# Kernel optimization log

Measured on AMD Instinct MI355X. Metric: run time of the kernel, lower is better.

The kernel has to match this reference:

```python
import jax, jax.numpy as jnp
import numpy as np


def setup_inputs() -> dict:
    key = jax.random.key(0)
    k1, k2 = jax.random.split(key)
    B, Lc, Lm, D = 8, 2048, 2048, 128
    context = jax.random.normal(k1, (B, Lc, D), dtype=jnp.float32)
    main = jax.random.normal(k2, (B, Lm, D), dtype=jnp.float32)
    return {"context": context, "main": main}


def reference(context, main):
    # weights[b,c,m] = sum_d context[b,c,d] * main[b,m,d]   (Keras dot axes=[2,2])
    weights = jnp.einsum("bcd,bmd->bcm", context, main)
    # K.softmax default axis=-1: normalize over the main-length axis m
    weights = jax.nn.softmax(weights, axis=-1)
    # dot([weights, context], axes=1): contract axis 1 (c) of both -> (B, Lm, D)
    weighted = jnp.einsum("bcm,bcd->bmd", weights, context)
    return main - weighted
```

## Files before the change

### kernel.cpp

```cpp
#include <hip/hip_runtime.h>


#define BATCH 8
#define L_SEQ 2048
#define DD 128
#define SHIFT 40.0f
#define LDA 136

typedef __attribute__((ext_vector_type(8))) short bf16x8;
typedef __attribute__((ext_vector_type(4))) short bf16x4;
typedef __attribute__((ext_vector_type(4))) float f32x4;
typedef __attribute__((ext_vector_type(16))) float f32x16;
typedef __attribute__((ext_vector_type(4))) unsigned int uint4v;

__device__ __forceinline__ short f2bf(float f) {
    unsigned u = __builtin_bit_cast(unsigned, f);
    return (short)((u + 0x8000u) >> 16);
}

__device__ __forceinline__ void gl2lds16(const short* g, short* l) {
    __builtin_amdgcn_global_load_lds(
        (const __attribute__((address_space(1))) unsigned int*)g,
        (__attribute__((address_space(3))) unsigned int*)l, 16, 0, 0);
}

template <int NT>
__device__ __forceinline__ void stage_tile(short* __restrict__ dst,
                                           const float* __restrict__ src,
                                           int nelts, int t) {
    for (int base = 0; base < nelts; base += NT * 8) {
        int flat = base + t * 8;
        const float4* p = (const float4*)(src + flat);
        float4 v0 = p[0];
        float4 v1 = p[1];
        bf16x8 s;
        s[0] = f2bf(v0.x); s[1] = f2bf(v0.y); s[2] = f2bf(v0.z); s[3] = f2bf(v0.w);
        s[4] = f2bf(v1.x); s[5] = f2bf(v1.y); s[6] = f2bf(v1.z); s[7] = f2bf(v1.w);
        int row = flat >> 7;
        int col = flat & 127;
        *(bf16x8*)&dst[row * LDA + col] = s;
    }
}

__global__ __launch_bounds__(256) void zero_kernel(float* __restrict__ p, int n) {
    int i = blockIdx.x * 256 + threadIdx.x;
    if (i < n) p[i] = 0.0f;
}


__global__ __launch_bounds__(256) void convert_kernel(const float* __restrict__ ctx,
                                                      const float* __restrict__ mn,
                                                      short* __restrict__ Cbf,
                                                      short* __restrict__ Mbf,
                                                      float* __restrict__ Lg) {
    int tid = blockIdx.x * 256 + threadIdx.x;
    if (tid < BATCH * L_SEQ) Lg[tid] = 0.0f;
    const int half = BATCH * L_SEQ * DD / 8;
    int id = tid;
    const float* src;
    short* dst;
    if (id < half) { src = ctx; dst = Cbf; }
    else           { id -= half; src = mn; dst = Mbf; }
    int row = id >> 4;
    int lc = id & 15;
    const float4* p = (const float4*)(src + ((size_t)row << 7) + lc * 8);
    float4 v0 = p[0];
    float4 v1 = p[1];
    bf16x8 s;
    s[0] = f2bf(v0.x); s[1] = f2bf(v0.y); s[2] = f2bf(v0.z); s[3] = f2bf(v0.w);
    s[4] = f2bf(v1.x); s[5] = f2bf(v1.y); s[6] = f2bf(v1.z); s[7] = f2bf(v1.w);
    int pc = (lc & 8) | ((lc ^ row) & 7);
    *(bf16x8*)&dst[((size_t)row << 7) + pc * 8] = s;
}

__global__ __launch_bounds__(256, 2) void stats_kernel(const short* __restrict__ Cbf,
                                                       const short* __restrict__ Mbf,
                                                       float* __restrict__ Lg) {
    __shared__ short Cs[128 * 128];
    __shared__ short Ms[2][64 * 128];

    int bid = blockIdx.x;
    int mc = bid & 3;
    int ct = (bid >> 2) & 15;
    int b  = bid >> 6;
    int t = threadIdx.x;
    int w = t >> 6;
    int l = t & 63;
    int a15 = l & 15;
    int q = l >> 4;
    int h = a15 & 7;
    int cw = (w & 1) * 64;
    int mw = (w >> 1) * 32;

    {
        const short* gC = Cbf + ((size_t)(b * L_SEQ + ct * 128)) * DD;
        const short* gM = Mbf + ((size_t)(b * L_SEQ + mc * 512)) * DD;
        #pragma unroll
        for (int ii = 0; ii < 8; ++ii) {
            int inst = w * 8 + ii;
            gl2lds16(gC + inst * 512 + l * 8, Cs + inst * 512);
        }
        #pragma unroll
        for (int ii = 0; ii < 4; ++ii) {
            int inst = w * 4 + ii;
            gl2lds16(gM + inst * 512 + l * 8, Ms[0] + inst * 512);
        }
    }

    __syncthreads();

    {
        const short* gM = Mbf + ((size_t)(b * L_SEQ + mc * 512 + 64)) * DD;
        #pragma unroll
        for (int ii = 0; ii < 4; ++ii) {
            int inst = w * 4 + ii;
            gl2lds16(gM + inst * 512 + l * 8, Ms[1] + inst * 512);
        }
    }

    bf16x8 af[4][4];
    #pragma unroll
    for (int ks = 0; ks < 4; ++ks) {
        int aoff = ((ks * 4 + q) ^ h) * 8;
        #pragma unroll
        for (int i = 0; i < 4; ++i)
            af[ks][i] = *(const bf16x8*)&Cs[(cw + i * 16 + a15) * 128 + aoff];
    }

    float ls[4][4] = {};

    for (int ms = 0; ms < 8; ++ms) {
        int bp = ms & 1;
        if (ms > 0) {
            __syncthreads();
            if (ms < 7) {
                const short* gM = Mbf + ((size_t)(b * L_SEQ + mc * 512 + (ms + 1) * 64)) * DD;
                #pragma unroll
                for (int ii = 0; ii < 4; ++ii) {
                    int inst = w * 4 + ii;
                    gl2lds16(gM + inst * 512 + l * 8, Ms[bp ^ 1] + inst * 512);
                }
            }
        }

        f32x4 acc[4][2];
        #pragma unroll
        for (int i = 0; i < 4; ++i)
            #pragma unroll
            for (int j = 0; j < 2; ++j) {
                f32x4 z = {0.f, 0.f, 0.f, 0.f};
                acc[i][j] = z;
            }
        #pragma unroll
        for (int ks = 0; ks < 4; ++ks) {
            int aoff = ((ks * 4 + q) ^ h) * 8;
            bf16x8 bv[2];
            #pragma unroll
            for (int j = 0; j < 2; ++j)
                bv[j] = *(const bf16x8*)&Ms[bp][(mw + j * 16 + a15) * 128 + aoff];
            #pragma unroll
            for (int i = 0; i < 4; ++i)
                #pragma unroll
                for (int j = 0; j < 2; ++j)
                    acc[i][j] = __builtin_amdgcn_mfma_f32_16x16x32_bf16(af[ks][i], bv[j], acc[i][j], 0, 0, 0);
        }

        #pragma unroll
        for (int j = 0; j < 2; ++j)
            #pragma unroll
            for (int i = 0; i < 4; ++i)
                #pragma unroll
                for (int r = 0; r < 4; ++r)
                    ls[i][r] += __expf(acc[i][j][r] - SHIFT);
    }

    #pragma unroll
    for (int i = 0; i < 4; ++i)
        #pragma unroll
        for (int r = 0; r < 4; ++r) {
            float v = ls[i][r];
            v += __shfl_xor(v, 1);
            v += __shfl_xor(v, 2);
            v += __shfl_xor(v, 4);
            v += __shfl_xor(v, 8);
            ls[i][r] = v;
        }
    if (a15 == 0) {
        #pragma unroll
        for (int i = 0; i < 4; ++i) {
            int c = ct * 128 + cw + i * 16 + q * 4;
            #pragma unroll
            for (int r = 0; r < 4; ++r)
                atomicAdd(&Lg[(size_t)b * L_SEQ + c + r], ls[i][r]);
        }
    }
}

__global__ __launch_bounds__(256) void prep_kernel(const float* __restrict__ ctx,
                                                   const float* __restrict__ Lg,
                                                   short* __restrict__ CtL) {
    __shared__ short Ts[128 * LDA];
    __shared__ float invLs[128];

    int b = blockIdx.x >> 4;
    int cc = blockIdx.x & 15;
    int t = threadIdx.x;

    if (t < 128) invLs[t] = 1.0f / Lg[(size_t)b * L_SEQ + cc * 128 + t];
    __syncthreads();

    const float* src = ctx + ((size_t)(b * L_SEQ + cc * 128)) * DD;
    #pragma unroll
    for (int i = 0; i < 8; ++i) {
        int flat = i * 2048 + t * 8;
        int r = flat >> 7;
        int c = flat & 127;
        const float4* p = (const float4*)(src + flat);
        float4 v0 = p[0];
        float4 v1 = p[1];
        float il = invLs[r];
        bf16x8 s;
        s[0] = f2bf(v0.x * il); s[1] = f2bf(v0.y * il); s[2] = f2bf(v0.z * il); s[3] = f2bf(v0.w * il);
        s[4] = f2bf(v1.x * il); s[5] = f2bf(v1.y * il); s[6] = f2bf(v1.z * il); s[7] = f2bf(v1.w * il);
        *(bf16x8*)&Ts[r * LDA + c] = s;
    }
    __syncthreads();

    int d = t >> 1;
    int ch = (t & 1) * 64;
    int key = d & 7;
    #pragma unroll
    for (int i = 0; i < 8; ++i) {
        int c = ch + i * 8;
        bf16x8 v;
        #pragma unroll
        for (int j = 0; j < 8; ++j) v[j] = Ts[(c + j) * LDA + d];
        int pc = cc * 16 + (ch >> 3) + (i ^ key);
        *(bf16x8*)&CtL[((size_t)(b * DD + d)) * L_SEQ + pc * 8] = v;
    }
}

__global__ __launch_bounds__(512, 2) void attend_fused(const short* __restrict__ Cbf,
                                                       const short* __restrict__ Mbf,
                                                       const short* __restrict__ CtL,
                                                       const float* __restrict__ mn,
                                                       float* __restrict__ out) {
    __shared__ __align__(16) char smem[131072];

    int bid = blockIdx.x;
    int mtile = bid & 31;
    int b = bid >> 5;
    int t = threadIdx.x;
    int w = t >> 6;
    int l = t & 63;
    int la = l & 31;
    int hi = l >> 5;
    int mg = w >> 2;
    int ch = w & 3;

    int m_glob = mtile * 64 + mg * 32 + la;

    bf16x8 mf[8];
    {
        const short* mrow = Mbf + ((size_t)(b * L_SEQ + m_glob)) * DD;
        int key = m_glob & 7;
        #pragma unroll
        for (int ks = 0; ks < 8; ++ks) {
            int lc = ks * 2 + hi;
            int pc = (lc & 8) | ((lc ^ key) & 7);
            mf[ks] = *(const bf16x8*)&mrow[pc * 8];
        }
    }

    auto stage = [&](int cs, int p) {
        short* Cw = (short*)(smem + p * 65536);
        short* Tw = (short*)(smem + p * 65536 + 32768);
        const short* gC = Cbf + ((size_t)(b * L_SEQ + cs * 128)) * DD;
        #pragma unroll
        for (int ii = 0; ii < 4; ++ii) {
            int inst = w * 4 + ii;
            gl2lds16(gC + inst * 512 + l * 8, Cw + inst * 512);
        }
        const short* gT = CtL + (size_t)b * DD * L_SEQ + (size_t)cs * 128;
        #pragma unroll
        for (int ii = 0; ii < 4; ++ii) {
            int inst = w * 4 + ii;
            int row = inst * 4 + (l >> 4);
            gl2lds16(gT + (size_t)row * L_SEQ + (l & 15) * 8, Tw + inst * 512);
        }
    };

    f32x16 o[4];
    #pragma unroll
    for (int dg = 0; dg < 4; ++dg)
        #pragma unroll
        for (int r = 0; r < 16; ++r) o[dg][r] = 0.0f;

    stage(0, 0);

    for (int cs = 0; cs < 16; ++cs) {
        int p = cs & 1;
        __syncthreads();
        if (cs < 15) stage(cs + 1, p ^ 1);

        const short* Cw = (const short*)(smem + p * 65536);
        const short* Tw = (const short*)(smem + p * 65536 + 32768);

        f32x16 s;
        #pragma unroll
        for (int r = 0; r < 16; ++r) s[r] = 0.0f;
        int crow = ch * 32 + la;
        int ckey = la & 7;
        #pragma unroll
        for (int ks = 0; ks < 8; ++ks) {
            int lc = ks * 2 + hi;
            int pc = (lc & 8) | ((lc ^ ckey) & 7);
            bf16x8 av = *(const bf16x8*)&Cw[crow * 128 + pc * 8];
            s = __builtin_amdgcn_mfma_f32_32x32x16_bf16(av, mf[ks], s, 0, 0, 0);
        }

        unsigned u[4][2];
        #pragma unroll
        for (int q = 0; q < 4; ++q)
            #pragma unroll
            for (int jj = 0; jj < 2; ++jj) {
                float e0 = __expf(s[q * 4 + jj * 2]     - SHIFT);
                float e1 = __expf(s[q * 4 + jj * 2 + 1] - SHIFT);
                u[q][jj] = ((unsigned)(unsigned short)f2bf(e1) << 16)
                         |  (unsigned)(unsigned short)f2bf(e0);
            }

        bf16x8 pa[2];
        #pragma unroll
        for (int ks2 = 0; ks2 < 2; ++ks2) {
            unsigned a0 = u[2 * ks2][0],     a1 = u[2 * ks2][1];
            unsigned b0 = u[2 * ks2 + 1][0], b1 = u[2 * ks2 + 1][1];
            unsigned a0p = (unsigned)__shfl_xor((int)a0, 32);
            unsigned a1p = (unsigned)__shfl_xor((int)a1, 32);
            unsigned b0p = (unsigned)__shfl_xor((int)b0, 32);
            unsigned b1p = (unsigned)__shfl_xor((int)b1, 32);
            uint4v pw;
            pw.x = hi ? b0p : a0;
            pw.y = hi ? b1p : a1;
            pw.z = hi ? b0  : a0p;
            pw.w = hi ? b1  : a1p;
            pa[ks2] = __builtin_bit_cast(bf16x8, pw);
        }

        #pragma unroll
        for (int dg = 0; dg < 4; ++dg) {
            int drow = dg * 32 + la;
            int dkey = drow & 7;
            #pragma unroll
            for (int ks2 = 0; ks2 < 2; ++ks2) {
                int lc2 = ch * 4 + ks2 * 2 + hi;
                int pc2 = (lc2 & 8) | ((lc2 ^ dkey) & 7);
                bf16x8 tv = *(const bf16x8*)&Tw[drow * 128 + pc2 * 8];
                o[dg] = __builtin_amdgcn_mfma_f32_32x32x16_bf16(tv, pa[ks2], o[dg], 0, 0, 0);
            }
        }
    }

    __syncthreads();
    float* red = (float*)smem;
    {
        float* base = red + w * 4096;
        #pragma unroll
        for (int dg = 0; dg < 4; ++dg)
            #pragma unroll
            for (int r = 0; r < 16; ++r) {
                int d = dg * 32 + (r & 3) + 8 * (r >> 2) + 4 * hi;
                base[d * 32 + la] = o[dg][r];
            }
    }
    __syncthreads();

    {
        int mg2 = t >> 8;
        int dq  = (t >> 5) & 7;
        int m   = t & 31;
        int m_out = mtile * 64 + mg2 * 32 + m;
        size_t gbase = ((size_t)(b * L_SEQ + m_out)) * DD + dq * 16;
        const float* r0 = red + (mg2 * 4 + 0) * 4096;
        const float* r1 = red + (mg2 * 4 + 1) * 4096;
        const float* r2 = red + (mg2 * 4 + 2) * 4096;
        const float* r3 = red + (mg2 * 4 + 3) * 4096;
        #pragma unroll
        for (int jq = 0; jq < 4; ++jq) {
            f32x4 v;
            #pragma unroll
            for (int e = 0; e < 4; ++e) {
                int idx = (dq * 16 + jq * 4 + e) * 32 + m;
                v[e] = r0[idx] + r1[idx] + r2[idx] + r3[idx];
            }
            f32x4 mv = *(const f32x4*)&mn[gbase + jq * 4];
            f32x4 ov;
            ov[0] = mv[0] - v[0]; ov[1] = mv[1] - v[1];
            ov[2] = mv[2] - v[2]; ov[3] = mv[3] - v[3];
            *(f32x4*)&out[gbase + jq * 4] = ov;
        }
    }
}


__global__ __launch_bounds__(256, 4) void stats_fb(const float* __restrict__ ctx,
                                                   const float* __restrict__ mn,
                                                   float* __restrict__ Lg) {
    __shared__ short Cs[64 * LDA];
    __shared__ short Ms[64 * LDA];

    int bid = blockIdx.x;
    int mc = bid & 3;
    int ct = (bid >> 2) & 31;
    int b  = bid >> 7;
    int t = threadIdx.x;
    int w = t >> 6;
    int l = t & 63;
    int a15 = l & 15;
    int q = l >> 4;

    stage_tile<256>(Cs, ctx + ((size_t)b * L_SEQ + ct * 64) * DD, 64 * DD, t);

    float ls[4] = {0.f, 0.f, 0.f, 0.f};
    for (int mt = 0; mt < 8; ++mt) {
        __syncthreads();
        int m0 = (mc * 8 + mt) * 64;
        stage_tile<256>(Ms, mn + ((size_t)b * L_SEQ + m0) * DD, 64 * DD, t);
        __syncthreads();

        f32x4 acc[4] = {{0.f,0.f,0.f,0.f},{0.f,0.f,0.f,0.f},{0.f,0.f,0.f,0.f},{0.f,0.f,0.f,0.f}};
        #pragma unroll
        for (int ks = 0; ks < 4; ++ks) {
            int k0 = ks * 32 + q * 8;
            bf16x8 a = *(const bf16x8*)&Cs[(w * 16 + a15) * LDA + k0];
            #pragma unroll
            for (int g = 0; g < 4; ++g) {
                bf16x8 bb = *(const bf16x8*)&Ms[(g * 16 + a15) * LDA + k0];
                acc[g] = __builtin_amdgcn_mfma_f32_16x16x32_bf16(a, bb, acc[g], 0, 0, 0);
            }
        }
        #pragma unroll
        for (int g = 0; g < 4; ++g)
            #pragma unroll
            for (int r = 0; r < 4; ++r)
                ls[r] += __expf(acc[g][r] - SHIFT);
    }

    #pragma unroll
    for (int r = 0; r < 4; ++r) {
        float v = ls[r];
        v += __shfl_xor(v, 1);
        v += __shfl_xor(v, 2);
        v += __shfl_xor(v, 4);
        v += __shfl_xor(v, 8);
        ls[r] = v;
    }
    if (a15 == 0) {
        int c = ct * 64 + w * 16 + q * 4;
        #pragma unroll
        for (int r = 0; r < 4; ++r)
            atomicAdd(&Lg[(size_t)b * L_SEQ + c + r], ls[r]);
    }
}

__global__ __launch_bounds__(1024, 4) void attend_fb(const float* __restrict__ ctx,
                                                     const float* __restrict__ mn,
                                                     const float* __restrict__ Lg,
                                                     float* __restrict__ out) {
    __shared__ short Mt[64 * LDA];
    __shared__ short Cs[128 * LDA];
    __shared__ short Ct[128 * LDA];
    __shared__ short Ps[64 * LDA];
    __shared__ float invLs[128];

    int bid = blockIdx.x;
    int mtile = bid & 31;
    int b = bid >> 5;
    int m0 = mtile * 64;
    int t = threadIdx.x;
    int w = t >> 6;
    int l = t & 63;
    int a15 = l & 15;
    int q = l >> 4;
    int mg = w & 3;
    int pg = w >> 2;

    stage_tile<1024>(Mt, mn + ((size_t)b * L_SEQ + m0) * DD, 64 * DD, t);

    f32x4 oacc[2] = {{0.f,0.f,0.f,0.f},{0.f,0.f,0.f,0.f}};

    for (int cs = 0; cs < 16; ++cs) {
        int c0 = cs * 128;
        __syncthreads();
        stage_tile<1024>(Cs, ctx + ((size_t)b * L_SEQ + c0) * DD, 128 * DD, t);
        if (t < 128) invLs[t] = 1.0f / Lg[(size_t)b * L_SEQ + c0 + t];
        __syncthreads();

        {
            int cc = t & 127;
            int d0 = (t >> 7) * 16;
            #pragma unroll
            for (int hh = 0; hh < 2; ++hh) {
                bf16x8 v = *(const bf16x8*)&Cs[cc * LDA + d0 + hh * 8];
                #pragma unroll
                for (int j = 0; j < 8; ++j)
                    Ct[(d0 + hh * 8 + j) * LDA + cc] = v[j];
            }
        }

        f32x4 sacc[2] = {{0.f,0.f,0.f,0.f},{0.f,0.f,0.f,0.f}};
        #pragma unroll
        for (int ks = 0; ks < 4; ++ks) {
            int k0 = ks * 32 + q * 8;
            bf16x8 a = *(const bf16x8*)&Mt[(mg * 16 + a15) * LDA + k0];
            #pragma unroll
            for (int g = 0; g < 2; ++g) {
                bf16x8 bb = *(const bf16x8*)&Cs[((pg * 2 + g) * 16 + a15) * LDA + k0];
                sacc[g] = __builtin_amdgcn_mfma_f32_16x16x32_bf16(a, bb, sacc[g], 0, 0, 0);
            }
        }
        #pragma unroll
        for (int g = 0; g < 2; ++g) {
            int cl = (pg * 2 + g) * 16 + a15;
            float il = invLs[cl];
            #pragma unroll
            for (int r = 0; r < 4; ++r) {
                float p = __expf(sacc[g][r] - SHIFT) * il;
                Ps[(mg * 16 + q * 4 + r) * LDA + cl] = f2bf(p);
            }
        }
        __syncthreads();

        #pragma unroll
        for (int ks = 0; ks < 4; ++ks) {
            int k0 = ks * 32 + q * 8;
            bf16x8 a = *(const bf16x8*)&Ps[(mg * 16 + a15) * LDA + k0];
            #pragma unroll
            for (int g = 0; g < 2; ++g) {
                bf16x8 bb = *(const bf16x8*)&Ct[((pg * 2 + g) * 16 + a15) * LDA + k0];
                oacc[g] = __builtin_amdgcn_mfma_f32_16x16x32_bf16(a, bb, oacc[g], 0, 0, 0);
            }
        }
    }

    #pragma unroll
    for (int g = 0; g < 2; ++g) {
        int dl = (pg * 2 + g) * 16 + a15;
        #pragma unroll
        for (int r = 0; r < 4; ++r) {
            int ml = mg * 16 + q * 4 + r;
            size_t idx = ((size_t)b * L_SEQ + m0 + ml) * DD + dl;
            out[idx] = mn[idx] - oacc[g][r];
        }
    }
}


extern "C" void kernel_launch(void* const* d_in, const int* in_sizes, int n_in,
                              void* d_out, int out_size, void* d_ws, size_t ws_size,
                              hipStream_t stream) {
    const float* ctx = (const float*)d_in[0];
    const float* mn  = (const float*)d_in[1];
    float* out = (float*)d_out;

    const size_t LG_BYTES = (size_t)BATCH * L_SEQ * sizeof(float);
    const size_t BF_BYTES = (size_t)BATCH * L_SEQ * DD * sizeof(short);
    const size_t NEED = LG_BYTES + 3 * BF_BYTES;

    float* Lg = (float*)d_ws;

    if (ws_size >= NEED) {
        short* Cbf = (short*)((char*)d_ws + LG_BYTES);
        short* Mbf = (short*)((char*)d_ws + LG_BYTES + BF_BYTES);
        short* CtL = (short*)((char*)d_ws + LG_BYTES + 2 * BF_BYTES);
        convert_kernel<<<2048, 256, 0, stream>>>(ctx, mn, Cbf, Mbf, Lg);
        stats_kernel<<<BATCH * 16 * 4, 256, 0, stream>>>(Cbf, Mbf, Lg);
        prep_kernel<<<BATCH * 16, 256, 0, stream>>>(ctx, Lg, CtL);
        attend_fused<<<BATCH * 32, 512, 0, stream>>>(Cbf, Mbf, CtL, mn, out);
    } else {
        int nL = BATCH * L_SEQ;
        zero_kernel<<<(nL + 255) / 256, 256, 0, stream>>>(Lg, nL);
        stats_fb<<<BATCH * 32 * 4, 256, 0, stream>>>(ctx, mn, Lg);
        attend_fb<<<BATCH * 32, 1024, 0, stream>>>(ctx, mn, Lg, out);
    }
}
```

Before: 119.2 us.

## Load attend operands directly from global memory and shrink attend blocks

The attend kernel stops staging context and transposed-context tiles through a double-buffered 128KB LDS pipeline. Each wave now reads its MFMA operands straight from global memory, relying on L2 and cache reuse. Blocks shrink to 256 threads covering 32 m rows, so the grid doubles and LDS use drops to the 64KB reduction buffer, which should raise occupancy and remove the per-iteration barriers. Block indices in both stats and attend are also remapped so the batch index varies fastest, spreading each batch's blocks across the chip. The cost is more global and cache traffic, since each wave loads the same C and T data independently, and load latency is exposed without explicit prefetch.

```diff
diff --git a/kernel.cpp b/kernel.cpp
--- a/kernel.cpp
+++ b/kernel.cpp
@@ -80,9 +80,10 @@
     __shared__ short Ms[2][64 * 128];
 
     int bid = blockIdx.x;
-    int mc = bid & 3;
-    int ct = (bid >> 2) & 15;
-    int b  = bid >> 6;
+    int b  = bid & 7;
+    int r2 = bid >> 3;
+    int mc = r2 & 3;
+    int ct = r2 >> 2;
     int t = threadIdx.x;
     int w = t >> 6;
     int l = t & 63;
@@ -240,55 +241,39 @@
     }
 }
 
-__global__ __launch_bounds__(512, 2) void attend_fused(const short* __restrict__ Cbf,
+__global__ __launch_bounds__(256, 2) void attend_fused(const short* __restrict__ Cbf,
                                                        const short* __restrict__ Mbf,
                                                        const short* __restrict__ CtL,
                                                        const float* __restrict__ mn,
                                                        float* __restrict__ out) {
-    __shared__ __align__(16) char smem[131072];
+    __shared__ float red[4][4096];
 
     int bid = blockIdx.x;
-    int mtile = bid & 31;
-    int b = bid >> 5;
+    int b = bid & 7;
+    int mtile = bid >> 3;
     int t = threadIdx.x;
     int w = t >> 6;
     int l = t & 63;
     int la = l & 31;
     int hi = l >> 5;
-    int mg = w >> 2;
-    int ch = w & 3;
-
-    int m_glob = mtile * 64 + mg * 32 + la;
+    int ch = w;
+
+    int m_glob = mtile * 32 + la;
+    int key7 = la & 7;
 
     bf16x8 mf[8];
     {
         const short* mrow = Mbf + ((size_t)(b * L_SEQ + m_glob)) * DD;
-        int key = m_glob & 7;
         #pragma unroll
         for (int ks = 0; ks < 8; ++ks) {
             int lc = ks * 2 + hi;
-            int pc = (lc & 8) | ((lc ^ key) & 7);
+            int pc = (lc & 8) | ((lc ^ key7) & 7);
             mf[ks] = *(const bf16x8*)&mrow[pc * 8];
         }
     }
 
-    auto stage = [&](int cs, int p) {
-        short* Cw = (short*)(smem + p * 65536);
-        short* Tw = (short*)(smem + p * 65536 + 32768);
-        const short* gC = Cbf + ((size_t)(b * L_SEQ + cs * 128)) * DD;
-        #pragma unroll
-        for (int ii = 0; ii < 4; ++ii) {
-            int inst = w * 4 + ii;
-            gl2lds16(gC + inst * 512 + l * 8, Cw + inst * 512);
-        }
-        const short* gT = CtL + (size_t)b * DD * L_SEQ + (size_t)cs * 128;
-        #pragma unroll
-        for (int ii = 0; ii < 4; ++ii) {
-            int inst = w * 4 + ii;
-            int row = inst * 4 + (l >> 4);
-            gl2lds16(gT + (size_t)row * L_SEQ + (l & 15) * 8, Tw + inst * 512);
-        }
-    };
+    const short* gC = Cbf + ((size_t)(b * L_SEQ + ch * 32 + la)) * DD;
+    const short* gT = CtL + ((size_t)(b * DD + la)) * L_SEQ;
 
     f32x16 o[4];
     #pragma unroll
@@ -296,26 +281,28 @@
         #pragma unroll
         for (int r = 0; r < 16; ++r) o[dg][r] = 0.0f;
 
-    stage(0, 0);
-
     for (int cs = 0; cs < 16; ++cs) {
-        int p = cs & 1;
-        __syncthreads();
-        if (cs < 15) stage(cs + 1, p ^ 1);
-
-        const short* Cw = (const short*)(smem + p * 65536);
-        const short* Tw = (const short*)(smem + p * 65536 + 32768);
+        const short* gCw = gC + (size_t)cs * 128 * DD;
+        const short* gTw = gT + cs * 128;
+
+        bf16x8 tv[4][2];
+        #pragma unroll
+        for (int dg = 0; dg < 4; ++dg)
+            #pragma unroll
+            for (int ks2 = 0; ks2 < 2; ++ks2) {
+                int lc2 = ch * 4 + ks2 * 2 + hi;
+                int pc2 = (lc2 & 8) | ((lc2 ^ key7) & 7);
+                tv[dg][ks2] = *(const bf16x8*)&gTw[(size_t)(dg * 32) * L_SEQ + pc2 * 8];
+            }
 
         f32x16 s;
         #pragma unroll
         for (int r = 0; r < 16; ++r) s[r] = 0.0f;
-        int crow = ch * 32 + la;
-        int ckey = la & 7;
         #pragma unroll
         for (int ks = 0; ks < 8; ++ks) {
             int lc = ks * 2 + hi;
-            int pc = (lc & 8) | ((lc ^ ckey) & 7);
-            bf16x8 av = *(const bf16x8*)&Cw[crow * 128 + pc * 8];
+            int pc = (lc & 8) | ((lc ^ key7) & 7);
+            bf16x8 av = *(const bf16x8*)&gCw[pc * 8];
             s = __builtin_amdgcn_mfma_f32_32x32x16_bf16(av, mf[ks], s, 0, 0, 0);
         }
 
@@ -348,23 +335,14 @@
         }
 
         #pragma unroll
-        for (int dg = 0; dg < 4; ++dg) {
-            int drow = dg * 32 + la;
-            int dkey = drow & 7;
-            #pragma unroll
-            for (int ks2 = 0; ks2 < 2; ++ks2) {
-                int lc2 = ch * 4 + ks2 * 2 + hi;
-                int pc2 = (lc2 & 8) | ((lc2 ^ dkey) & 7);
-                bf16x8 tv = *(const bf16x8*)&Tw[drow * 128 + pc2 * 8];
-                o[dg] = __builtin_amdgcn_mfma_f32_32x32x16_bf16(tv, pa[ks2], o[dg], 0, 0, 0);
-            }
-        }
-    }
-
-    __syncthreads();
-    float* red = (float*)smem;
+        for (int dg = 0; dg < 4; ++dg)
+            #pragma unroll
+            for (int ks2 = 0; ks2 < 2; ++ks2)
+                o[dg] = __builtin_amdgcn_mfma_f32_32x32x16_bf16(tv[dg][ks2], pa[ks2], o[dg], 0, 0, 0);
+    }
+
     {
-        float* base = red + w * 4096;
+        float* base = red[w];
         #pragma unroll
         for (int dg = 0; dg < 4; ++dg)
             #pragma unroll
@@ -376,22 +354,16 @@
     __syncthreads();
 
     {
-        int mg2 = t >> 8;
-        int dq  = (t >> 5) & 7;
-        int m   = t & 31;
-        int m_out = mtile * 64 + mg2 * 32 + m;
-        size_t gbase = ((size_t)(b * L_SEQ + m_out)) * DD + dq * 16;
-        const float* r0 = red + (mg2 * 4 + 0) * 4096;
-        const float* r1 = red + (mg2 * 4 + 1) * 4096;
-        const float* r2 = red + (mg2 * 4 + 2) * 4096;
-        const float* r3 = red + (mg2 * 4 + 3) * 4096;
+        int m  = t & 31;
+        int dq = t >> 5;
+        size_t gbase = ((size_t)(b * L_SEQ + mtile * 32 + m)) * DD + dq * 16;
         #pragma unroll
         for (int jq = 0; jq < 4; ++jq) {
             f32x4 v;
             #pragma unroll
             for (int e = 0; e < 4; ++e) {
                 int idx = (dq * 16 + jq * 4 + e) * 32 + m;
-                v[e] = r0[idx] + r1[idx] + r2[idx] + r3[idx];
+                v[e] = red[0][idx] + red[1][idx] + red[2][idx] + red[3][idx];
             }
             f32x4 mv = *(const f32x4*)&mn[gbase + jq * 4];
             f32x4 ov;
@@ -576,7 +548,7 @@
         convert_kernel<<<2048, 256, 0, stream>>>(ctx, mn, Cbf, Mbf, Lg);
         stats_kernel<<<BATCH * 16 * 4, 256, 0, stream>>>(Cbf, Mbf, Lg);
         prep_kernel<<<BATCH * 16, 256, 0, stream>>>(ctx, Lg, CtL);
-        attend_fused<<<BATCH * 32, 512, 0, stream>>>(Cbf, Mbf, CtL, mn, out);
+        attend_fused<<<BATCH * 64, 256, 0, stream>>>(Cbf, Mbf, CtL, mn, out);
     } else {
         int nL = BATCH * L_SEQ;
         zero_kernel<<<(nL + 255) / 256, 256, 0, stream>>>(Lg, nL);
```

Result: slower. 124.9 us (+4.8%).

## Prefetch two stages ahead with partial vmcnt waits and batch-major block order

Applied to the files above, without the earlier changes.

Both the stats and attend kernels now issue global-to-LDS loads two tiles ahead. Each iteration waits with an explicit s_waitcnt vmcnt on only the oldest outstanding loads instead of a full __syncthreads drain, and the freed buffer is refilled after a barrier at the end of the iteration. Block indices are remapped so the batch index varies fastest, which changes how concurrently running blocks share L2 data. This aims to hide more load latency behind MFMA work, but it relies on exact counts of outstanding vector-memory operations and adds an extra barrier per iteration.

```diff
diff --git a/kernel.cpp b/kernel.cpp
--- a/kernel.cpp
+++ b/kernel.cpp
@@ -23,6 +23,10 @@
         (const __attribute__((address_space(1))) unsigned int*)g,
         (__attribute__((address_space(3))) unsigned int*)l, 16, 0, 0);
 }
+
+__device__ __forceinline__ void waitv8() { asm volatile("s_waitcnt vmcnt(8)" ::: "memory"); }
+__device__ __forceinline__ void waitv4() { asm volatile("s_waitcnt vmcnt(4)" ::: "memory"); }
+__device__ __forceinline__ void waitv0() { asm volatile("s_waitcnt vmcnt(0)" ::: "memory"); }
 
 template <int NT>
 __device__ __forceinline__ void stage_tile(short* __restrict__ dst,
@@ -80,9 +84,10 @@
     __shared__ short Ms[2][64 * 128];
 
     int bid = blockIdx.x;
-    int mc = bid & 3;
-    int ct = (bid >> 2) & 15;
-    int b  = bid >> 6;
+    int b  = bid & 7;
+    int r2 = bid >> 3;
+    int mc = r2 & 3;
+    int ct = r2 >> 2;
     int t = threadIdx.x;
     int w = t >> 6;
     int l = t & 63;
@@ -92,9 +97,10 @@
     int cw = (w & 1) * 64;
     int mw = (w >> 1) * 32;
 
+    const short* gC = Cbf + ((size_t)(b * L_SEQ + ct * 128)) * DD;
+    const short* gM = Mbf + ((size_t)(b * L_SEQ + mc * 512)) * DD;
+
     {
-        const short* gC = Cbf + ((size_t)(b * L_SEQ + ct * 128)) * DD;
-        const short* gM = Mbf + ((size_t)(b * L_SEQ + mc * 512)) * DD;
         #pragma unroll
         for (int ii = 0; ii < 8; ++ii) {
             int inst = w * 8 + ii;
@@ -105,18 +111,16 @@
             int inst = w * 4 + ii;
             gl2lds16(gM + inst * 512 + l * 8, Ms[0] + inst * 512);
         }
-    }
-
-    __syncthreads();
-
-    {
-        const short* gM = Mbf + ((size_t)(b * L_SEQ + mc * 512 + 64)) * DD;
         #pragma unroll
         for (int ii = 0; ii < 4; ++ii) {
             int inst = w * 4 + ii;
-            gl2lds16(gM + inst * 512 + l * 8, Ms[1] + inst * 512);
-        }
-    }
+            gl2lds16(gM + (size_t)64 * DD + inst * 512 + l * 8, Ms[1] + inst * 512);
+        }
+    }
+
+    waitv8();
+    __builtin_amdgcn_s_barrier();
+    __builtin_amdgcn_sched_barrier(0);
 
     bf16x8 af[4][4];
     #pragma unroll
@@ -131,17 +135,9 @@
 
     for (int ms = 0; ms < 8; ++ms) {
         int bp = ms & 1;
-        if (ms > 0) {
-            __syncthreads();
-            if (ms < 7) {
-                const short* gM = Mbf + ((size_t)(b * L_SEQ + mc * 512 + (ms + 1) * 64)) * DD;
-                #pragma unroll
-                for (int ii = 0; ii < 4; ++ii) {
-                    int inst = w * 4 + ii;
-                    gl2lds16(gM + inst * 512 + l * 8, Ms[bp ^ 1] + inst * 512);
-                }
-            }
-        }
+        if (ms < 7) waitv4(); else waitv0();
+        __builtin_amdgcn_s_barrier();
+        __builtin_amdgcn_sched_barrier(0);
 
         f32x4 acc[4][2];
         #pragma unroll
@@ -172,6 +168,17 @@
                 #pragma unroll
                 for (int r = 0; r < 4; ++r)
                     ls[i][r] += __expf(acc[i][j][r] - SHIFT);
+
+        __builtin_amdgcn_s_barrier();
+        __builtin_amdgcn_sched_barrier(0);
+        if (ms + 2 < 8) {
+            #pragma unroll
+            for (int ii = 0; ii < 4; ++ii) {
+                int inst = w * 4 + ii;
+                gl2lds16(gM + (size_t)(ms + 2) * 64 * DD + inst * 512 + l * 8,
+                         Ms[bp] + inst * 512);
+            }
+        }
     }
 
     #pragma unroll
@@ -248,8 +255,8 @@
     __shared__ __align__(16) char smem[131072];
 
     int bid = blockIdx.x;
-    int mtile = bid & 31;
-    int b = bid >> 5;
+    int b = bid & 7;
+    int mtile = bid >> 3;
     int t = threadIdx.x;
     int w = t >> 6;
     int l = t & 63;
@@ -259,15 +266,15 @@
     int ch = w & 3;
 
     int m_glob = mtile * 64 + mg * 32 + la;
+    int key7 = la & 7;
 
     bf16x8 mf[8];
     {
         const short* mrow = Mbf + ((size_t)(b * L_SEQ + m_glob)) * DD;
-        int key = m_glob & 7;
         #pragma unroll
         for (int ks = 0; ks < 8; ++ks) {
             int lc = ks * 2 + hi;
-            int pc = (lc & 8) | ((lc ^ key) & 7);
+            int pc = (lc & 8) | ((lc ^ key7) & 7);
             mf[ks] = *(const bf16x8*)&mrow[pc * 8];
         }
     }
@@ -297,11 +304,13 @@
         for (int r = 0; r < 16; ++r) o[dg][r] = 0.0f;
 
     stage(0, 0);
+    stage(1, 1);
 
     for (int cs = 0; cs < 16; ++cs) {
         int p = cs & 1;
-        __syncthreads();
-        if (cs < 15) stage(cs + 1, p ^ 1);
+        if (cs < 15) waitv8(); else waitv0();
+        __builtin_amdgcn_s_barrier();
+        __builtin_amdgcn_sched_barrier(0);
 
         const short* Cw = (const short*)(smem + p * 65536);
         const short* Tw = (const short*)(smem + p * 65536 + 32768);
@@ -310,11 +319,10 @@
         #pragma unroll
         for (int r = 0; r < 16; ++r) s[r] = 0.0f;
         int crow = ch * 32 + la;
-        int ckey = la & 7;
         #pragma unroll
         for (int ks = 0; ks < 8; ++ks) {
             int lc = ks * 2 + hi;
-            int pc = (lc & 8) | ((lc ^ ckey) & 7);
+            int pc = (lc & 8) | ((lc ^ key7) & 7);
             bf16x8 av = *(const bf16x8*)&Cw[crow * 128 + pc * 8];
             s = __builtin_amdgcn_mfma_f32_32x32x16_bf16(av, mf[ks], s, 0, 0, 0);
         }
@@ -350,15 +358,18 @@
         #pragma unroll
         for (int dg = 0; dg < 4; ++dg) {
             int drow = dg * 32 + la;
-            int dkey = drow & 7;
             #pragma unroll
             for (int ks2 = 0; ks2 < 2; ++ks2) {
                 int lc2 = ch * 4 + ks2 * 2 + hi;
-                int pc2 = (lc2 & 8) | ((lc2 ^ dkey) & 7);
+                int pc2 = (lc2 & 8) | ((lc2 ^ key7) & 7);
                 bf16x8 tv = *(const bf16x8*)&Tw[drow * 128 + pc2 * 8];
                 o[dg] = __builtin_amdgcn_mfma_f32_32x32x16_bf16(tv, pa[ks2], o[dg], 0, 0, 0);
             }
         }
+
+        __builtin_amdgcn_s_barrier();
+        __builtin_amdgcn_sched_barrier(0);
+        if (cs + 2 < 16) stage(cs + 2, p);
     }
 
     __syncthreads();
```

New measurement: 119.1 us. About the same (-0.1%).
